# Optimization experiments

Hardware: AMD Instinct MI355X
Metric: run time of the kernel (lower is better)

## Reference

```python
import jax, jax.numpy as jnp
import numpy as np

B, L, D = 16, 512, 128
EPS = 1e-12


def _newton_schulz_1(S):
    # One Newton-Schulz orthogonalization iteration on batched [B,D,D] matrices:
    # X = S/||S||_F ; X <- 1.5*X - 0.5 * X @ X^T @ X
    norm = jnp.sqrt(jnp.sum(S * S, axis=(-2, -1), keepdims=True)) + 1e-6
    X = S / norm
    XXtX = jnp.einsum('bij,bkj,bkl->bil', X, X, X)
    return 1.5 * X - 0.5 * XXtX


def _poly(v, coeffs):
    # PolynomialFeatureLayer, degree 2, dimension-preserving:
    # phi(v) = c0*v + c1*v^2
    return coeffs[0] * v + coeffs[1] * v * v


def setup_inputs() -> dict:
    key = jax.random.key(0)
    ks = jax.random.split(key, 6)
    s = 1.0 / np.sqrt(D)
    x = jax.random.normal(ks[0], (B, L, D), jnp.float32)
    Wq = jax.random.normal(ks[1], (D, D), jnp.float32) * s
    Wk = jax.random.normal(ks[2], (D, D), jnp.float32) * s
    Wout = jax.random.normal(ks[3], (D, D), jnp.float32) * s
    bout = jnp.zeros((D,), jnp.float32)
    M0 = jax.random.normal(ks[4], (D, D), jnp.float32) * 0.01   # M_init
    S0 = jnp.zeros((D, D), jnp.float32)                          # S_init
    P0 = jnp.eye(D, dtype=jnp.float32) * 0.01                    # P_init
    log_gain = jnp.zeros((D,), jnp.float32)                      # QKProjectionLayer gain
    coeffs = jnp.array([1.0, 0.5], jnp.float32)                  # poly coeffs
    return {"x": x, "Wq": Wq, "Wk": Wk, "P0": P0, "M0": M0, "S0": S0,
            "log_gain": log_gain, "coeffs": coeffs, "Wout": Wout, "bout": bout}


def reference(x, Wq, Wk, P0, M0, S0, log_gain, coeffs, Wout, bout):
    b, l, d = x.shape
    q = jnp.einsum('bld,ed->ble', x, Wq)                 # q_proj (no bias)
    k = jnp.einsum('bld,ed->ble', x, Wk)                 # k_proj (no bias)
    k = k / jnp.maximum(jnp.linalg.norm(k, axis=-1, keepdims=True), EPS)  # F.normalize

    # QKProjectionLayer: rotate q by per-batch projection P, tanh gate with learned gain
    P = jnp.broadcast_to(P0, (b, d, d))
    gain = jnp.exp(log_gain)
    q_aligned = jnp.tanh(gain * jnp.einsum('bld,bde->ble', q, P))
    # (P_new = 0.99*P + 0.01*mean_t outer(q,k); state only, unused by output)

    k_phi = _poly(k, coeffs)
    q_phi = _poly(q_aligned, coeffs)

    M = jnp.broadcast_to(M0, (b, d, d))
    S = jnpp = jnp.broadcast_to(S0, (b, d, d))

    def step(carry, inputs):
        M, S = carry
        k_t, q_t, x_t = inputs                           # each [B,D]
        pred = jnp.einsum('bde,be->bd', M, k_t)
        err = pred - x_t
        S = 0.9 * S + err[:, :, None] * k_t[:, None, :]  # outer-product grad
        S_ortho = _newton_schulz_1(S)
        M = 0.99 * M - 0.01 * S_ortho
        y_t = jnp.einsum('bde,be->bd', M, q_t)
        return (M, S), y_t

    xs = (jnp.swapaxes(k_phi, 0, 1), jnp.swapaxes(q_phi, 0, 1), jnp.swapaxes(x, 0, 1))
    (_, _), ys = jax.lax.scan(step, (M, S), xs)          # ys: [L,B,D]
    stacked = jnp.swapaxes(ys, 0, 1)                     # [B,L,D]
    out = jnp.einsum('bld,ed->ble', stacked, Wout) + bout  # out_proj
    return out
```

## Files before the change

### kernel.cpp

```cpp
#include <hip/hip_runtime.h>

#define BB 16
#define LL 512
#define DD 128
#define CH 16
#define NCH (LL / CH)

typedef float v2f __attribute__((ext_vector_type(2)));
__device__ __forceinline__ v2f mk2(float x, float y) { v2f r; r.x = x; r.y = y; return r; }
__device__ __forceinline__ v2f fma2(v2f a, v2f b, v2f c) {
    return __builtin_elementwise_fma(a, b, c);
}

__device__ __forceinline__ float red8(float v) {
    v += __int_as_float(__builtin_amdgcn_update_dpp(
            0, __float_as_int(v), 0xB1, 0xF, 0xF, true));
    v += __int_as_float(__builtin_amdgcn_update_dpp(
            0, __float_as_int(v), 0x4E, 0xF, 0xF, true));
    v += __int_as_float(__builtin_amdgcn_update_dpp(
            0, __float_as_int(v), 0x141, 0xF, 0xF, true));
    return v;
}

#define SCAN_REGS __attribute__((amdgpu_waves_per_eu(2, 2)))

__global__ void transpose3_kernel(const float* __restrict__ Wq,
                                  const float* __restrict__ Wk,
                                  const float* __restrict__ Wout,
                                  float* __restrict__ WqT,
                                  float* __restrict__ WkT,
                                  float* __restrict__ WoutT) {
    const float* src; float* dst;
    if (blockIdx.x == 0)      { src = Wq;   dst = WqT;   }
    else if (blockIdx.x == 1) { src = Wk;   dst = WkT;   }
    else                      { src = Wout; dst = WoutT; }
    for (int idx = threadIdx.x; idx < DD * DD; idx += blockDim.x) {
        int r = idx >> 7, c = idx & 127;
        dst[c * DD + r] = src[idx];
    }
}

__global__ __launch_bounds__(128) void prologue_kernel(
        const float* __restrict__ x, const float* __restrict__ WqT,
        const float* __restrict__ WkT, const float* __restrict__ P0,
        const float* __restrict__ log_gain, const float* __restrict__ coeffs,
        float* __restrict__ kphi, float* __restrict__ qphi,
        float* __restrict__ cvt) {
    const int row0 = blockIdx.x * 8;
    const int e = threadIdx.x;
    __shared__ float xs[8][DD];
    __shared__ float qrow[8][DD];
    __shared__ float wred[8][2];
    __shared__ float cvred[8][2];

    #pragma unroll
    for (int rr = 0; rr < 8; ++rr)
        xs[rr][e] = x[(size_t)(row0 + rr) * DD + e];
    __syncthreads();

    float aq[8] = {0,0,0,0,0,0,0,0}, ak[8] = {0,0,0,0,0,0,0,0};
    #pragma unroll 4
    for (int d = 0; d < DD; ++d) {
        float wq = WqT[d * DD + e];
        float wk = WkT[d * DD + e];
        #pragma unroll
        for (int rr = 0; rr < 8; ++rr) {
            float xv = xs[rr][d];
            aq[rr] = fmaf(xv, wq, aq[rr]);
            ak[rr] = fmaf(xv, wk, ak[rr]);
        }
    }
    const int lane = threadIdx.x & 63, wv = threadIdx.x >> 6;
    #pragma unroll
    for (int rr = 0; rr < 8; ++rr) {
        float s = ak[rr] * ak[rr];
        #pragma unroll
        for (int m = 1; m <= 32; m <<= 1) s += __shfl_xor(s, m);
        if (lane == 0) wred[rr][wv] = s;
    }
    __syncthreads();
    const float c0 = coeffs[0], c1v = coeffs[1];
    #pragma unroll
    for (int rr = 0; rr < 8; ++rr) {
        float s = wred[rr][0] + wred[rr][1];
        float kn = ak[rr] / fmaxf(sqrtf(s), 1e-12f);
        float kv = c0 * kn + c1v * kn * kn;
        kphi[(size_t)(row0 + rr) * DD + e] = kv;
        float sq = kv * kv;
        #pragma unroll
        for (int m = 1; m <= 32; m <<= 1) sq += __shfl_xor(sq, m);
        if (lane == 0) cvred[rr][wv] = sq;
        qrow[rr][e] = aq[rr];
    }
    __syncthreads();
    if (e < 8) cvt[row0 + e] = cvred[e][0] + cvred[e][1];
    float acc[8] = {0,0,0,0,0,0,0,0};
    #pragma unroll 4
    for (int d = 0; d < DD; ++d) {
        float pv = P0[d * DD + e];
        #pragma unroll
        for (int rr = 0; rr < 8; ++rr) acc[rr] = fmaf(qrow[rr][d], pv, acc[rr]);
    }
    const float g = expf(log_gain[e]);
    #pragma unroll
    for (int rr = 0; rr < 8; ++rr) {
        float qa = tanhf(g * acc[rr]);
        qphi[(size_t)(row0 + rr) * DD + e] = c0 * qa + c1v * qa * qa;
    }
}


#define SCAN_STEP(SL, KKT, KKN)                                               \
  {                                                                           \
    const int so = (SL) * DD;                                                 \
    const float4 ft0 = *(const float4*)&ftab[(SL)][0];                        \
    const float4 ft1 = *(const float4*)&ftab[(SL)][4];                        \
    float4 pre0, pre1, pre2;                                                  \
    const bool doPre = ((SL) == 0) && (tc + 1 < NCH);                         \
    if (doPre) {                                                              \
      const size_t nbg = base + (size_t)(tc + 1) * CH * DD;                   \
      {                                                                       \
        int seg = w * 3 + 0, arr = seg >> 3, sub = seg & 7;                   \
        pre0 = *(const float4*)((arr == 0 ? kphi : (arr == 1 ? qphi : x))     \
                                + nbg + sub * 256 + lane * 4);                \
      }                                                                       \
      {                                                                       \
        int seg = w * 3 + 1, arr = seg >> 3, sub = seg & 7;                   \
        pre1 = *(const float4*)((arr == 0 ? kphi : (arr == 1 ? qphi : x))     \
                                + nbg + sub * 256 + lane * 4);                \
      }                                                                       \
      {                                                                       \
        int seg = w * 3 + 2, arr = seg >> 3, sub = seg & 7;                   \
        pre2 = *(const float4*)((arr == 0 ? kphi : (arr == 1 ? qphi : x))     \
                                + nbg + sub * 256 + lane * 4);                \
      }                                                                       \
    }                                                                         \
    v2f uu2[8], pa2[8];                                                       \
    {                                                                         \
      const float4* u4 = (const float4*)us;                                   \
      const float4* p4 = (const float4*)ps;                                   \
      _Pragma("unroll")                                                       \
      for (int m = 0; m < 4; ++m) {                                           \
        float4 a4 = u4[j + 8 * m], b4 = p4[j + 8 * m];                        \
        uu2[2*m]     = mk2(a4.x, a4.y);                                       \
        uu2[2*m + 1] = mk2(a4.z, a4.w);                                       \
        pa2[2*m]     = mk2(b4.x, b4.y);                                       \
        pa2[2*m + 1] = mk2(b4.z, b4.w);                                       \
      }                                                                       \
    }                                                                         \
    const float2 vc = *(const float2*)&kcb[so + r0];                          \
    const float vcxs = vc.x * ft0.y, vcys = vc.y * ft0.y;                     \
    const v2f vcx = mk2(vcxs, vcxs), vcy = mk2(vcys, vcys);                   \
    v2f w0v = mk2(0.f, 0.f), w1v = mk2(0.f, 0.f);                             \
    v2f h0v = mk2(0.f, 0.f), h1v = mk2(0.f, 0.f);                             \
    v2f cuv = mk2(0.f, 0.f), cupv = mk2(0.f, 0.f);                            \
    _Pragma("unroll")                                                         \
    for (int p = 0; p < 8; ++p) {                                             \
      v2f uv = uu2[p], pv = pa2[p];                                           \
      v2f st0 = ST2[p], st1 = ST2[8 + p];                                     \
      w0v  = fma2(st0, uv, w0v);                                              \
      w1v  = fma2(st1, uv, w1v);                                              \
      h0v  = fma2(st0, pv, h0v);                                              \
      h1v  = fma2(st1, pv, h1v);                                              \
      cuv  = fma2(uv, uv, cuv);                                               \
      cupv = fma2(uv, pv, cupv);                                              \
      ST2[p]     = fma2(vcx, uv, st0);                                        \
      ST2[8 + p] = fma2(vcy, uv, st1);                                        \
    }                                                                         \
    float w0 = red8(ft0.x * (w0v.x + w0v.y));                                 \
    float w1 = red8(ft0.x * (w1v.x + w1v.y));                                 \
    float h0 = red8(ft0.x * (h0v.x + h0v.y));                                 \
    float h1 = red8(ft0.x * (h1v.x + h1v.y));                                 \
    const float cu  = red8(cuv.x + cuv.y);                                    \
    const float cup = red8(cupv.x + cupv.y);                                  \
    n2 = a2v * n2 + 2.0f * a * cup + cu * cv;                                 \
       \
    const float nrm  = sqrtf(fmaxf(n2, 0.f)) + 1e-6f;                         \
    const float rn   = 1.0f / nrm;                                            \
    const float rn3  = rn * rn * rn;                                          \
    const float c1s  = rn * ft1.x;                                            \
    const float c2s  = rn3 * ft1.y;                                           \
    if (j == 0) {                                                             \
      *(float2*)&wsv[r0] = make_float2(w0, w1);                               \
      *(float2*)&hs[r0]  = make_float2(h0, h1);                               \
    }                                                                         \
    if (doPre) {                                                              \
      float* kn = kc[cb ^ 1]; float* qn = qc[cb ^ 1]; float* xn = xc[cb ^ 1]; \
      {                                                                       \
        int seg = w * 3 + 0, arr = seg >> 3, sub = seg & 7;                   \
        *(float4*)((arr == 0 ? kn : (arr == 1 ? qn : xn))                     \
                   + sub * 256 + lane * 4) = pre0;                            \
      }                                                                       \
      {                                                                       \
        int seg = w * 3 + 1, arr = seg >> 3, sub = seg & 7;                   \
        *(float4*)((arr == 0 ? kn : (arr == 1 ? qn : xn))                     \
                   + sub * 256 + lane * 4) = pre1;                            \
      }                                                                       \
      {                                                                       \
        int seg = w * 3 + 2, arr = seg >> 3, sub = seg & 7;                   \
        *(float4*)((arr == 0 ? kn : (arr == 1 ? qn : xn))                     \
                   + sub * 256 + lane * 4) = pre2;                            \
      }                                                                       \
    }                                                                         \
    __syncthreads();                                                          \
       \
    const float cvN = cvt[(size_t)b * LL + (size_t)(tc * CH + (SL) + 1)];     \
    v2f ww2[8];                                                               \
    v2f g0v = mk2(0.f, 0.f), g1v = mk2(0.f, 0.f);                             \
    {                                                                         \
      const float4* w4 = (const float4*)wsv;                                  \
      _Pragma("unroll")                                                       \
      for (int m = 0; m < 4; ++m) {                                           \
        float4 a4 = w4[j + 8 * m];                                            \
        v2f wv0 = mk2(a4.x, a4.y), wv1 = mk2(a4.z, a4.w);                     \
        ww2[2*m] = wv0; ww2[2*m + 1] = wv1;                                   \
        g0v = fma2(S2[2*m],     wv0, g0v);                                    \
        g0v = fma2(S2[2*m + 1], wv1, g0v);                                    \
        g1v = fma2(S2[8 + 2*m],     wv0, g1v);                                \
        g1v = fma2(S2[8 + 2*m + 1], wv1, g1v);                                \
      }                                                                       \
    }                                                                         \
    float g0 = red8(ft0.x * (g0v.x + g0v.y));                                 \
    float g1 = red8(ft0.x * (g1v.x + g1v.y));                                 \
    const float rho0 = a2v * g0 + a * cu * p0 + (a * cup + cv * cu) * u0;     \
    const float rho1 = a2v * g1 + a * cu * p1 + (a * cup + cv * cu) * u1;     \
    const float sg0  = a2v * p0 + a * cv * u0;                                \
    const float sg1  = a2v * p1 + a * cv * u1;                                \
    const float ta0  = a2v * u0, ta1 = a2v * u1;                              \
    const float f3i  = ft0.w;                                                 \
    const float u0p  = u0 * ft0.y, u1p = u1 * ft0.y;                          \
    const v2f u0v = mk2(u0p, u0p), u1v = mk2(u1p, u1p);                       \
    const v2f r0v = mk2(rho0 * f3i, rho0 * f3i);                              \
    const v2f r1v = mk2(rho1 * f3i, rho1 * f3i);                              \
    const v2f s0v = mk2(sg0 * f3i, sg0 * f3i);                                \
    const v2f s1v = mk2(sg1 * f3i, sg1 * f3i);                                \
    const v2f t0v = mk2(ta0 * f3i, ta0 * f3i);                                \
    const v2f t1v = mk2(ta1 * f3i, ta1 * f3i);                                \
    const v2f c1p = mk2(c1s, c1s), c2p = mk2(c2s, c2s);                       \
    const float* knb = ((SL) + 1 < CH) ? (kcb + so + DD) : kc[cb ^ 1];        \
    const float* xnb = ((SL) + 1 < CH) ? (xcb + so + DD) : xc[cb ^ 1];        \
    v2f y0v = mk2(0.f, 0.f), y1v = mk2(0.f, 0.f);                             \
    v2f pr0n = mk2(0.f, 0.f), pr1n = mk2(0.f, 0.f);                           \
    v2f pp0n = mk2(0.f, 0.f), pp1n = mk2(0.f, 0.f);                           \
    {                                                                         \
      const float4* h4  = (const float4*)hs;                                  \
      const float4* q4  = (const float4*)(qcb + so);                          \
      const float4* k4n = (const float4*)knb;                                 \
      _Pragma("unroll")                                                       \
      for (int m = 0; m < 4; ++m) {                                           \
        float4 b4  = h4[j + 8 * m];                                           \
        float4 c4v = q4[j + 8 * m];                                           \
        float4 k4v = k4n[j + 8 * m];                                          \
        v2f hv0 = mk2(b4.x, b4.y),   hv1 = mk2(b4.z, b4.w);                   \
        v2f qv0 = mk2(c4v.x, c4v.y), qv1 = mk2(c4v.z, c4v.w);                 \
        v2f kn0 = mk2(k4v.x, k4v.y), kn1 = mk2(k4v.z, k4v.w);                 \
        KKN[2*m] = kn0; KKN[2*m + 1] = kn1;                                   \
        v2f wv0 = ww2[2*m], wv1 = ww2[2*m + 1];                               \
        v2f kv0 = KKT[2*m], kv1 = KKT[2*m + 1];                               \
        v2f sn0 = fma2(u0v, kv0, S2[2*m]);                                    \
        v2f sn1 = fma2(u0v, kv1, S2[2*m + 1]);                                \
        S2[2*m] = sn0; S2[2*m + 1] = sn1;                                     \
        v2f an0 = fma2(r0v, kv0, fma2(s0v, wv0, fma2(t0v, hv0, A2[2*m])));    \
        v2f an1 = fma2(r0v, kv1, fma2(s0v, wv1, fma2(t0v, hv1, A2[2*m + 1])));\
        A2[2*m] = an0; A2[2*m + 1] = an1;                                     \
        v2f mn0 = fma2(c1p, sn0, fma2(c2p, an0, M2[2*m]));                    \
        v2f mn1 = fma2(c1p, sn1, fma2(c2p, an1, M2[2*m + 1]));                \
        M2[2*m] = mn0; M2[2*m + 1] = mn1;                                     \
        y0v  = fma2(mn0, qv0, y0v);                                           \
        y0v  = fma2(mn1, qv1, y0v);                                           \
        pr0n = fma2(mn0, kn0, pr0n);                                          \
        pr0n = fma2(mn1, kn1, pr0n);                                          \
        pp0n = fma2(sn0, kn0, pp0n);                                          \
        pp0n = fma2(sn1, kn1, pp0n);                                          \
        v2f sm0 = fma2(u1v, kv0, S2[8 + 2*m]);                                \
        v2f sm1 = fma2(u1v, kv1, S2[8 + 2*m + 1]);                            \
        S2[8 + 2*m] = sm0; S2[8 + 2*m + 1] = sm1;                             \
        v2f am0 = fma2(r1v, kv0, fma2(s1v, wv0, fma2(t1v, hv0, A2[8 + 2*m])));\
        v2f am1 = fma2(r1v, kv1,                                              \
                       fma2(s1v, wv1, fma2(t1v, hv1, A2[8 + 2*m + 1])));      \
        A2[8 + 2*m] = am0; A2[8 + 2*m + 1] = am1;                             \
        v2f mm0 = fma2(c1p, sm0, fma2(c2p, am0, M2[8 + 2*m]));                \
        v2f mm1 = fma2(c1p, sm1, fma2(c2p, am1, M2[8 + 2*m + 1]));            \
        M2[8 + 2*m] = mm0; M2[8 + 2*m + 1] = mm1;                             \
        y1v  = fma2(mm0, qv0, y1v);                                           \
        y1v  = fma2(mm1, qv1, y1v);                                           \
        pr1n = fma2(mm0, kn0, pr1n);                                          \
        pr1n = fma2(mm1, kn1, pr1n);                                          \
        pp1n = fma2(sm0, kn0, pp1n);                                          \
        pp1n = fma2(sm1, kn1, pp1n);                                          \
      }                                                                       \
    }                                                                         \
    float y0 = red8(ft1.z * (y0v.x + y0v.y));                                 \
    float y1 = red8(ft1.z * (y1v.x + y1v.y));                                 \
    if (j == 0)                                                               \
      *(float2*)&yc[so + r0] = make_float2(y0, y1);                           \
    const float2 xn = *(const float2*)&xnb[r0];                               \
    u0 = red8(fmaf(ft1.z, pr0n.x + pr0n.y, -0.125f * xn.x));                  \
    u1 = red8(fmaf(ft1.z, pr1n.x + pr1n.y, -0.125f * xn.y));                  \
    p0 = red8(ft0.z * (pp0n.x + pp0n.y));                                     \
    p1 = red8(ft0.z * (pp1n.x + pp1n.y));                                     \
    cv = cvN;                                                                 \
    if (j == 0) {                                                             \
      *(float2*)&us[r0] = make_float2(u0, u1);                                \
      *(float2*)&ps[r0] = make_float2(p0, p1);                                \
    }                                                                         \
    __syncthreads();                                                          \
  }

__global__ SCAN_REGS __launch_bounds__(512)
void scan_kernel(
        const float* __restrict__ kphi, const float* __restrict__ qphi,
        const float* __restrict__ x, const float* __restrict__ M0,
        const float* __restrict__ S0, float* __restrict__ ys,
        const float* __restrict__ cvt) {
    const int b    = blockIdx.x;
    const int tid  = threadIdx.x;
    const int j    = tid & 7;
    const int g    = tid >> 3;
    const int r0   = 2 * g;
    const int w    = tid >> 6;
    const int lane = tid & 63;

    __shared__ __align__(16) float kc[2][CH * DD];
    __shared__ __align__(16) float qc[2][CH * DD];
    __shared__ __align__(16) float xc[2][CH * DD];
    __shared__ __align__(16) float yc[CH * DD];
    __shared__ __align__(16) float us[DD], ps[DD], wsv[DD], hs[DD];
    __shared__ __align__(16) float ftab[CH][8];
    __shared__ float red[64];
    __shared__ float n2sh;

    {
        const float ia  = 1.0f / 0.9f;
        const float ia3 = ia * ia * ia;
        const float ra  = 0.9f / 0.99f;
        const float ra3 = 0.729f / 0.99f;
        float faS = 1.f, faiS = 1.f, fa3iS = 1.f;
        float q1S = -0.015f, q3S = 0.005f, fmS = 1.f;
        #pragma unroll 1
        for (int s = 0; s < CH; ++s) {
            float faN = faS * 0.9f;
            faiS *= ia; fa3iS *= ia3; q1S *= ra; q3S *= ra3; fmS *= 0.99f;
            if (tid == 0) {
                ftab[s][0] = faS;   ftab[s][1] = faiS;
                ftab[s][2] = faN;   ftab[s][3] = fa3iS;
                ftab[s][4] = q1S;   ftab[s][5] = q3S;
                ftab[s][6] = fmS;   ftab[s][7] = 0.f;
            }
            faS = faN;
        }
    }
    const float a2c = 0.9f * 0.9f, a4c = a2c * a2c, a8c = a4c * a4c;
    const float fa16 = a8c * a8c;
    const float fa48 = fa16 * fa16 * fa16;
    const float p2c = 0.99f * 0.99f, p4c = p2c * p2c, p8c = p4c * p4c;
    const float pm16 = p8c * p8c;

    v2f S2[16], ST2[16], A2[16], M2[16];
    {
        const float4* S04 = (const float4*)S0;
        const float4* M04 = (const float4*)M0;
        #pragma unroll
        for (int rl = 0; rl < 2; ++rl)
            #pragma unroll
            for (int m = 0; m < 4; ++m) {
                int f4 = (r0 + rl) * 32 + j + 8 * m;
                float4 s4 = S04[f4], m4 = M04[f4];
                int p = rl * 8 + 2 * m;
                S2[p]     = mk2(s4.x, s4.y);
                S2[p + 1] = mk2(s4.z, s4.w);
                M2[p]     = mk2(m4.x, m4.y);
                M2[p + 1] = mk2(m4.z, m4.w);
            }
        #pragma unroll
        for (int rl = 0; rl < 2; ++rl)
            #pragma unroll
            for (int m = 0; m < 4; ++m) {
                int p = rl * 8 + 2 * m;
                ST2[p]     = mk2(S0[(size_t)(4*j + 32*m + 0) * DD + r0 + rl],
                                 S0[(size_t)(4*j + 32*m + 1) * DD + r0 + rl]);
                ST2[p + 1] = mk2(S0[(size_t)(4*j + 32*m + 2) * DD + r0 + rl],
                                 S0[(size_t)(4*j + 32*m + 3) * DD + r0 + rl]);
            }
        #pragma unroll
        for (int p = 0; p < 16; ++p) A2[p] = mk2(0.f, 0.f);
    }

    float sp = 0.f;
    #pragma unroll
    for (int p = 0; p < 16; ++p) {
        sp = fmaf(S2[p].x, S2[p].x, sp);
        sp = fmaf(S2[p].y, S2[p].y, sp);
    }
    sp = red8(sp);
    if (j == 0) red[g] = sp;

    const size_t base = (size_t)b * LL * DD;

    #pragma unroll
    for (int i = 0; i < 3; ++i) {
        int seg = w * 3 + i, arr = seg >> 3, sub = seg & 7;
        const float* sp0 = (arr == 0 ? kphi : (arr == 1 ? qphi : x))
                           + base + sub * 256 + lane * 4;
        float* dp = (arr == 0 ? kc[0] : (arr == 1 ? qc[0] : xc[0]))
                    + sub * 256 + lane * 4;
        *(float4*)dp = *(const float4*)sp0;
    }
    __syncthreads();
    if (tid < 64) {
        float s = red[tid];
        #pragma unroll
        for (int m = 1; m <= 32; m <<= 1) s += __shfl_xor(s, m);
        if (tid == 0) n2sh = s;
    }
    __syncthreads();
    float n2 = n2sh;

    const float a = 0.9f, a2v = 0.81f;

    v2f kk2[8], kkn[8];
    float u0, u1, p0, p1, cv;
    {
        const float4* k4 = (const float4*)kc[0];
        v2f pr0v = mk2(0.f, 0.f), pr1v = mk2(0.f, 0.f);
        v2f pp0v = mk2(0.f, 0.f), pp1v = mk2(0.f, 0.f);
        v2f cvv  = mk2(0.f, 0.f);
        #pragma unroll
        for (int m = 0; m < 4; ++m) {
            float4 v4 = k4[j + 8 * m];
            v2f k0 = mk2(v4.x, v4.y), k1 = mk2(v4.z, v4.w);
            kk2[2*m] = k0; kk2[2*m + 1] = k1;
            pr0v = fma2(M2[2*m],     k0, pr0v);
            pr0v = fma2(M2[2*m + 1], k1, pr0v);
            pr1v = fma2(M2[8 + 2*m],     k0, pr1v);
            pr1v = fma2(M2[8 + 2*m + 1], k1, pr1v);
            pp0v = fma2(S2[2*m],     k0, pp0v);
            pp0v = fma2(S2[2*m + 1], k1, pp0v);
            pp1v = fma2(S2[8 + 2*m],     k0, pp1v);
            pp1v = fma2(S2[8 + 2*m + 1], k1, pp1v);
            cvv  = fma2(k0, k0, cvv);
            cvv  = fma2(k1, k1, cvv);
        }
        float pr0 = red8(pr0v.x + pr0v.y);
        float pr1 = red8(pr1v.x + pr1v.y);
        p0 = red8(pp0v.x + pp0v.y);
        p1 = red8(pp1v.x + pp1v.y);
        cv = red8(cvv.x + cvv.y);
        const float2 xv = *(const float2*)&xc[0][r0];
        u0 = pr0 - xv.x; u1 = pr1 - xv.y;
        if (j == 0) {
            *(float2*)&us[r0] = make_float2(u0, u1);
            *(float2*)&ps[r0] = make_float2(p0, p1);
        }
    }
    __syncthreads();

    #pragma unroll 1
    for (int tc = 0; tc < NCH; ++tc) {
        const int cb = tc & 1;
        const float* kcb = kc[cb];
        const float* qcb = qc[cb];
        const float* xcb = xc[cb];

        #pragma unroll 1
        for (int sl2 = 0; sl2 < CH; sl2 += 2) {
            SCAN_STEP(sl2,     kk2, kkn)
            SCAN_STEP(sl2 + 1, kkn, kk2)
        }

        float4 yv = *(float4*)&yc[tid * 4];
        *(float4*)(ys + base + (size_t)tc * CH * DD + tid * 4) = yv;

        if (tc + 1 < NCH) {
            const v2f rs = mk2(fa16, fa16);
            const v2f rA = mk2(fa48, fa48);
            const v2f rM = mk2(pm16, pm16);
            #pragma unroll
            for (int p = 0; p < 16; ++p) {
                S2[p] *= rs; ST2[p] *= rs; A2[p] *= rA; M2[p] *= rM;
            }
        }
    }
}

#undef SCAN_STEP

__global__ __launch_bounds__(128) void epilogue_kernel(
        const float* __restrict__ ys, const float* __restrict__ WoutT,
        const float* __restrict__ bout, float* __restrict__ out) {
    const int row0 = blockIdx.x * 8;
    const int e = threadIdx.x;
    __shared__ float yr[8][DD];
    #pragma unroll
    for (int rr = 0; rr < 8; ++rr)
        yr[rr][e] = ys[(size_t)(row0 + rr) * DD + e];
    __syncthreads();
    float acc[8] = {0,0,0,0,0,0,0,0};
    #pragma unroll 4
    for (int d = 0; d < DD; ++d) {
        float w = WoutT[d * DD + e];
        #pragma unroll
        for (int rr = 0; rr < 8; ++rr) acc[rr] = fmaf(yr[rr][d], w, acc[rr]);
    }
    const float bo = bout[e];
    #pragma unroll
    for (int rr = 0; rr < 8; ++rr)
        out[(size_t)(row0 + rr) * DD + e] = acc[rr] + bo;
}

extern "C" void kernel_launch(void* const* d_in, const int* in_sizes, int n_in,
                              void* d_out, int out_size, void* d_ws, size_t ws_size,
                              hipStream_t stream) {
    const float* x        = (const float*)d_in[0];
    const float* Wq       = (const float*)d_in[1];
    const float* Wk       = (const float*)d_in[2];
    const float* P0       = (const float*)d_in[3];
    const float* M0       = (const float*)d_in[4];
    const float* S0       = (const float*)d_in[5];
    const float* log_gain = (const float*)d_in[6];
    const float* coeffs   = (const float*)d_in[7];
    const float* Wout     = (const float*)d_in[8];
    const float* bout     = (const float*)d_in[9];
    float* out = (float*)d_out;

    float* ws    = (float*)d_ws;
    float* WqT   = ws;
    float* WkT   = ws + 16384;
    float* WoutT = ws + 32768;
    float* kphi  = ws + 49152;
    float* qphi  = kphi + (size_t)BB * LL * DD;
    float* ysb   = qphi + (size_t)BB * LL * DD;
    float* cvt   = ysb  + (size_t)BB * LL * DD;

    hipLaunchKernelGGL(transpose3_kernel, dim3(3), dim3(256), 0, stream,
                       Wq, Wk, Wout, WqT, WkT, WoutT);
    hipLaunchKernelGGL(prologue_kernel, dim3(BB * LL / 8), dim3(128), 0, stream,
                       x, WqT, WkT, P0, log_gain, coeffs, kphi, qphi, cvt);
    hipLaunchKernelGGL(scan_kernel, dim3(BB), dim3(512), 0, stream,
                       kphi, qphi, x, M0, S0, ysb, cvt);
    hipLaunchKernelGGL(epilogue_kernel, dim3(BB * LL / 8), dim3(128), 0, stream,
                       ysb, WoutT, bout, out);
}
```

Baseline: 1.062 ms.

## Halve scan block size, give each thread four state rows

The scan kernel now runs 256 threads per batch instead of 512, and each thread owns four rows of the S, ST, A and M state instead of two. The per-step loops, reductions, prefetch segments and ys stores are rewritten to match, and the waves-per-EU hint drops to 1 so more registers are available. The goal is to cut barrier and shared-memory exchange cost per step and to get more instruction-level parallelism per lane. In exchange, register pressure doubles, which risks spills, and fewer waves are left to hide latency.

```diff
diff --git a/kernel.cpp b/kernel.cpp
--- a/kernel.cpp
+++ b/kernel.cpp
@@ -22,7 +22,7 @@
     return v;
 }
 
-#define SCAN_REGS __attribute__((amdgpu_waves_per_eu(2, 2)))
+#define SCAN_REGS __attribute__((amdgpu_waves_per_eu(1, 1)))
 
 __global__ void transpose3_kernel(const float* __restrict__ Wq,
                                   const float* __restrict__ Wk,
@@ -115,24 +115,15 @@
     const int so = (SL) * DD;                                                 \
     const float4 ft0 = *(const float4*)&ftab[(SL)][0];                        \
     const float4 ft1 = *(const float4*)&ftab[(SL)][4];                        \
-    float4 pre0, pre1, pre2;                                                  \
+    float4 pre[6];                                                            \
     const bool doPre = ((SL) == 0) && (tc + 1 < NCH);                         \
     if (doPre) {                                                              \
       const size_t nbg = base + (size_t)(tc + 1) * CH * DD;                   \
-      {                                                                       \
-        int seg = w * 3 + 0, arr = seg >> 3, sub = seg & 7;                   \
-        pre0 = *(const float4*)((arr == 0 ? kphi : (arr == 1 ? qphi : x))     \
-                                + nbg + sub * 256 + lane * 4);                \
-      }                                                                       \
-      {                                                                       \
-        int seg = w * 3 + 1, arr = seg >> 3, sub = seg & 7;                   \
-        pre1 = *(const float4*)((arr == 0 ? kphi : (arr == 1 ? qphi : x))     \
-                                + nbg + sub * 256 + lane * 4);                \
-      }                                                                       \
-      {                                                                       \
-        int seg = w * 3 + 2, arr = seg >> 3, sub = seg & 7;                   \
-        pre2 = *(const float4*)((arr == 0 ? kphi : (arr == 1 ? qphi : x))     \
-                                + nbg + sub * 256 + lane * 4);                \
+      _Pragma("unroll")                                                       \
+      for (int i = 0; i < 6; ++i) {                                           \
+        int seg = w * 6 + i, arr = seg >> 3, sub = seg & 7;                   \
+        pre[i] = *(const float4*)((arr == 0 ? kphi : (arr == 1 ? qphi : x))   \
+                                  + nbg + sub * 256 + lane * 4);              \
       }                                                                       \
     }                                                                         \
     v2f uu2[8], pa2[8];                                                       \
@@ -148,65 +139,63 @@
         pa2[2*m + 1] = mk2(b4.z, b4.w);                                       \
       }                                                                       \
     }                                                                         \
-    const float2 vc = *(const float2*)&kcb[so + r0];                          \
-    const float vcxs = vc.x * ft0.y, vcys = vc.y * ft0.y;                     \
-    const v2f vcx = mk2(vcxs, vcxs), vcy = mk2(vcys, vcys);                   \
-    v2f w0v = mk2(0.f, 0.f), w1v = mk2(0.f, 0.f);                             \
-    v2f h0v = mk2(0.f, 0.f), h1v = mk2(0.f, 0.f);                             \
+    const float4 vc = *(const float4*)&kcb[so + r0];                          \
+    v2f vcb[4];                                                               \
+    vcb[0] = mk2(vc.x * ft0.y, vc.x * ft0.y);                                 \
+    vcb[1] = mk2(vc.y * ft0.y, vc.y * ft0.y);                                 \
+    vcb[2] = mk2(vc.z * ft0.y, vc.z * ft0.y);                                 \
+    vcb[3] = mk2(vc.w * ft0.y, vc.w * ft0.y);                                 \
+    v2f wAv[4], hAv[4];                                                       \
+    _Pragma("unroll")                                                         \
+    for (int rl = 0; rl < 4; ++rl) { wAv[rl] = mk2(0.f, 0.f);                 \
+                                     hAv[rl] = mk2(0.f, 0.f); }               \
     v2f cuv = mk2(0.f, 0.f), cupv = mk2(0.f, 0.f);                            \
     _Pragma("unroll")                                                         \
     for (int p = 0; p < 8; ++p) {                                             \
       v2f uv = uu2[p], pv = pa2[p];                                           \
-      v2f st0 = ST2[p], st1 = ST2[8 + p];                                     \
-      w0v  = fma2(st0, uv, w0v);                                              \
-      w1v  = fma2(st1, uv, w1v);                                              \
-      h0v  = fma2(st0, pv, h0v);                                              \
-      h1v  = fma2(st1, pv, h1v);                                              \
+      _Pragma("unroll")                                                       \
+      for (int rl = 0; rl < 4; ++rl) {                                        \
+        v2f st = ST2[rl*8 + p];                                               \
+        wAv[rl] = fma2(st, uv, wAv[rl]);                                      \
+        hAv[rl] = fma2(st, pv, hAv[rl]);                                      \
+        ST2[rl*8 + p] = fma2(vcb[rl], uv, st);                                \
+      }                                                                       \
       cuv  = fma2(uv, uv, cuv);                                               \
       cupv = fma2(uv, pv, cupv);                                              \
-      ST2[p]     = fma2(vcx, uv, st0);                                        \
-      ST2[8 + p] = fma2(vcy, uv, st1);                                        \
-    }                                                                         \
-    float w0 = red8(ft0.x * (w0v.x + w0v.y));                                 \
-    float w1 = red8(ft0.x * (w1v.x + w1v.y));                                 \
-    float h0 = red8(ft0.x * (h0v.x + h0v.y));                                 \
-    float h1 = red8(ft0.x * (h1v.x + h1v.y));                                 \
+    }                                                                         \
+    float wr[4], hr[4];                                                       \
+    _Pragma("unroll")                                                         \
+    for (int rl = 0; rl < 4; ++rl) {                                          \
+      wr[rl] = red8(ft0.x * (wAv[rl].x + wAv[rl].y));                         \
+      hr[rl] = red8(ft0.x * (hAv[rl].x + hAv[rl].y));                         \
+    }                                                                         \
     const float cu  = red8(cuv.x + cuv.y);                                    \
     const float cup = red8(cupv.x + cupv.y);                                  \
     n2 = a2v * n2 + 2.0f * a * cup + cu * cv;                                 \
-       \
     const float nrm  = sqrtf(fmaxf(n2, 0.f)) + 1e-6f;                         \
     const float rn   = 1.0f / nrm;                                            \
     const float rn3  = rn * rn * rn;                                          \
     const float c1s  = rn * ft1.x;                                            \
     const float c2s  = rn3 * ft1.y;                                           \
     if (j == 0) {                                                             \
-      *(float2*)&wsv[r0] = make_float2(w0, w1);                               \
-      *(float2*)&hs[r0]  = make_float2(h0, h1);                               \
+      *(float4*)&wsv[r0] = make_float4(wr[0], wr[1], wr[2], wr[3]);           \
+      *(float4*)&hs[r0]  = make_float4(hr[0], hr[1], hr[2], hr[3]);           \
     }                                                                         \
     if (doPre) {                                                              \
       float* kn = kc[cb ^ 1]; float* qn = qc[cb ^ 1]; float* xn = xc[cb ^ 1]; \
-      {                                                                       \
-        int seg = w * 3 + 0, arr = seg >> 3, sub = seg & 7;                   \
+      _Pragma("unroll")                                                       \
+      for (int i = 0; i < 6; ++i) {                                           \
+        int seg = w * 6 + i, arr = seg >> 3, sub = seg & 7;                   \
         *(float4*)((arr == 0 ? kn : (arr == 1 ? qn : xn))                     \
-                   + sub * 256 + lane * 4) = pre0;                            \
+                   + sub * 256 + lane * 4) = pre[i];                          \
       }                                                                       \
-      {                                                                       \
-        int seg = w * 3 + 1, arr = seg >> 3, sub = seg & 7;                   \
-        *(float4*)((arr == 0 ? kn : (arr == 1 ? qn : xn))                     \
-                   + sub * 256 + lane * 4) = pre1;                            \
-      }                                                                       \
-      {                                                                       \
-        int seg = w * 3 + 2, arr = seg >> 3, sub = seg & 7;                   \
-        *(float4*)((arr == 0 ? kn : (arr == 1 ? qn : xn))                     \
-                   + sub * 256 + lane * 4) = pre2;                            \
-      }                                                                       \
     }                                                                         \
     __syncthreads();                                                          \
-       \
     const float cvN = cvt[(size_t)b * LL + (size_t)(tc * CH + (SL) + 1)];     \
     v2f ww2[8];                                                               \
-    v2f g0v = mk2(0.f, 0.f), g1v = mk2(0.f, 0.f);                             \
+    v2f gAv[4];                                                               \
+    _Pragma("unroll")                                                         \
+    for (int rl = 0; rl < 4; ++rl) gAv[rl] = mk2(0.f, 0.f);                   \
     {                                                                         \
       const float4* w4 = (const float4*)wsv;                                  \
       _Pragma("unroll")                                                       \
@@ -214,34 +203,35 @@
         float4 a4 = w4[j + 8 * m];                                            \
         v2f wv0 = mk2(a4.x, a4.y), wv1 = mk2(a4.z, a4.w);                     \
         ww2[2*m] = wv0; ww2[2*m + 1] = wv1;                                   \
-        g0v = fma2(S2[2*m],     wv0, g0v);                                    \
-        g0v = fma2(S2[2*m + 1], wv1, g0v);                                    \
-        g1v = fma2(S2[8 + 2*m],     wv0, g1v);                                \
-        g1v = fma2(S2[8 + 2*m + 1], wv1, g1v);                                \
+        _Pragma("unroll")                                                     \
+        for (int rl = 0; rl < 4; ++rl) {                                      \
+          gAv[rl] = fma2(S2[rl*8 + 2*m],     wv0, gAv[rl]);                   \
+          gAv[rl] = fma2(S2[rl*8 + 2*m + 1], wv1, gAv[rl]);                   \
+        }                                                                     \
       }                                                                       \
     }                                                                         \
-    float g0 = red8(ft0.x * (g0v.x + g0v.y));                                 \
-    float g1 = red8(ft0.x * (g1v.x + g1v.y));                                 \
-    const float rho0 = a2v * g0 + a * cu * p0 + (a * cup + cv * cu) * u0;     \
-    const float rho1 = a2v * g1 + a * cu * p1 + (a * cup + cv * cu) * u1;     \
-    const float sg0  = a2v * p0 + a * cv * u0;                                \
-    const float sg1  = a2v * p1 + a * cv * u1;                                \
-    const float ta0  = a2v * u0, ta1 = a2v * u1;                              \
-    const float f3i  = ft0.w;                                                 \
-    const float u0p  = u0 * ft0.y, u1p = u1 * ft0.y;                          \
-    const v2f u0v = mk2(u0p, u0p), u1v = mk2(u1p, u1p);                       \
-    const v2f r0v = mk2(rho0 * f3i, rho0 * f3i);                              \
-    const v2f r1v = mk2(rho1 * f3i, rho1 * f3i);                              \
-    const v2f s0v = mk2(sg0 * f3i, sg0 * f3i);                                \
-    const v2f s1v = mk2(sg1 * f3i, sg1 * f3i);                                \
-    const v2f t0v = mk2(ta0 * f3i, ta0 * f3i);                                \
-    const v2f t1v = mk2(ta1 * f3i, ta1 * f3i);                                \
+    const float f3i = ft0.w;                                                  \
+    v2f uB[4], rB[4], sB[4], tB[4];                                           \
+    _Pragma("unroll")                                                         \
+    for (int rl = 0; rl < 4; ++rl) {                                          \
+      float gr  = red8(ft0.x * (gAv[rl].x + gAv[rl].y));                      \
+      float rho = a2v * gr + a * cu * p_[rl] + (a * cup + cv * cu) * u_[rl];  \
+      float sg  = a2v * p_[rl] + a * cv * u_[rl];                             \
+      float ta  = a2v * u_[rl];                                               \
+      uB[rl] = mk2(u_[rl] * ft0.y, u_[rl] * ft0.y);                           \
+      rB[rl] = mk2(rho * f3i, rho * f3i);                                     \
+      sB[rl] = mk2(sg * f3i, sg * f3i);                                       \
+      tB[rl] = mk2(ta * f3i, ta * f3i);                                       \
+    }                                                                         \
     const v2f c1p = mk2(c1s, c1s), c2p = mk2(c2s, c2s);                       \
     const float* knb = ((SL) + 1 < CH) ? (kcb + so + DD) : kc[cb ^ 1];        \
     const float* xnb = ((SL) + 1 < CH) ? (xcb + so + DD) : xc[cb ^ 1];        \
-    v2f y0v = mk2(0.f, 0.f), y1v = mk2(0.f, 0.f);                             \
-    v2f pr0n = mk2(0.f, 0.f), pr1n = mk2(0.f, 0.f);                           \
-    v2f pp0n = mk2(0.f, 0.f), pp1n = mk2(0.f, 0.f);                           \
+    v2f yv[4], prv[4], ppv[4];                                                \
+    _Pragma("unroll")                                                         \
+    for (int rl = 0; rl < 4; ++rl) {                                          \
+      yv[rl] = mk2(0.f, 0.f); prv[rl] = mk2(0.f, 0.f);                        \
+      ppv[rl] = mk2(0.f, 0.f);                                                \
+    }                                                                         \
     {                                                                         \
       const float4* h4  = (const float4*)hs;                                  \
       const float4* q4  = (const float4*)(qcb + so);                          \
@@ -257,57 +247,55 @@
         KKN[2*m] = kn0; KKN[2*m + 1] = kn1;                                   \
         v2f wv0 = ww2[2*m], wv1 = ww2[2*m + 1];                               \
         v2f kv0 = KKT[2*m], kv1 = KKT[2*m + 1];                               \
-        v2f sn0 = fma2(u0v, kv0, S2[2*m]);                                    \
-        v2f sn1 = fma2(u0v, kv1, S2[2*m + 1]);                                \
-        S2[2*m] = sn0; S2[2*m + 1] = sn1;                                     \
-        v2f an0 = fma2(r0v, kv0, fma2(s0v, wv0, fma2(t0v, hv0, A2[2*m])));    \
-        v2f an1 = fma2(r0v, kv1, fma2(s0v, wv1, fma2(t0v, hv1, A2[2*m + 1])));\
-        A2[2*m] = an0; A2[2*m + 1] = an1;                                     \
-        v2f mn0 = fma2(c1p, sn0, fma2(c2p, an0, M2[2*m]));                    \
-        v2f mn1 = fma2(c1p, sn1, fma2(c2p, an1, M2[2*m + 1]));                \
-        M2[2*m] = mn0; M2[2*m + 1] = mn1;                                     \
-        y0v  = fma2(mn0, qv0, y0v);                                           \
-        y0v  = fma2(mn1, qv1, y0v);                                           \
-        pr0n = fma2(mn0, kn0, pr0n);                                          \
-        pr0n = fma2(mn1, kn1, pr0n);                                          \
-        pp0n = fma2(sn0, kn0, pp0n);                                          \
-        pp0n = fma2(sn1, kn1, pp0n);                                          \
-        v2f sm0 = fma2(u1v, kv0, S2[8 + 2*m]);                                \
-        v2f sm1 = fma2(u1v, kv1, S2[8 + 2*m + 1]);                            \
-        S2[8 + 2*m] = sm0; S2[8 + 2*m + 1] = sm1;                             \
-        v2f am0 = fma2(r1v, kv0, fma2(s1v, wv0, fma2(t1v, hv0, A2[8 + 2*m])));\
-        v2f am1 = fma2(r1v, kv1,                                              \
-                       fma2(s1v, wv1, fma2(t1v, hv1, A2[8 + 2*m + 1])));      \
-        A2[8 + 2*m] = am0; A2[8 + 2*m + 1] = am1;                             \
-        v2f mm0 = fma2(c1p, sm0, fma2(c2p, am0, M2[8 + 2*m]));                \
-        v2f mm1 = fma2(c1p, sm1, fma2(c2p, am1, M2[8 + 2*m + 1]));            \
-        M2[8 + 2*m] = mm0; M2[8 + 2*m + 1] = mm1;                             \
-        y1v  = fma2(mm0, qv0, y1v);                                           \
-        y1v  = fma2(mm1, qv1, y1v);                                           \
-        pr1n = fma2(mm0, kn0, pr1n);                                          \
-        pr1n = fma2(mm1, kn1, pr1n);                                          \
-        pp1n = fma2(sm0, kn0, pp1n);                                          \
-        pp1n = fma2(sm1, kn1, pp1n);                                          \
+        _Pragma("unroll")                                                     \
+        for (int rl = 0; rl < 4; ++rl) {                                      \
+          v2f sn0 = fma2(uB[rl], kv0, S2[rl*8 + 2*m]);                        \
+          v2f sn1 = fma2(uB[rl], kv1, S2[rl*8 + 2*m + 1]);                    \
+          S2[rl*8 + 2*m] = sn0; S2[rl*8 + 2*m + 1] = sn1;                     \
+          v2f an0 = fma2(rB[rl], kv0,                                         \
+                         fma2(sB[rl], wv0, fma2(tB[rl], hv0,                  \
+                                                A2[rl*8 + 2*m])));            \
+          v2f an1 = fma2(rB[rl], kv1,                                         \
+                         fma2(sB[rl], wv1, fma2(tB[rl], hv1,                  \
+                                                A2[rl*8 + 2*m + 1])));        \
+          A2[rl*8 + 2*m] = an0; A2[rl*8 + 2*m + 1] = an1;                     \
+          v2f mn0 = fma2(c1p, sn0, fma2(c2p, an0, M2[rl*8 + 2*m]));           \
+          v2f mn1 = fma2(c1p, sn1, fma2(c2p, an1, M2[rl*8 + 2*m + 1]));       \
+          M2[rl*8 + 2*m] = mn0; M2[rl*8 + 2*m + 1] = mn1;                     \
+          yv[rl]  = fma2(mn0, qv0, yv[rl]);                                   \
+          yv[rl]  = fma2(mn1, qv1, yv[rl]);                                   \
+          prv[rl] = fma2(mn0, kn0, prv[rl]);                                  \
+          prv[rl] = fma2(mn1, kn1, prv[rl]);                                  \
+          ppv[rl] = fma2(sn0, kn0, ppv[rl]);                                  \
+          ppv[rl] = fma2(sn1, kn1, ppv[rl]);                                  \
+        }                                                                     \
       }                                                                       \
     }                                                                         \
-    float y0 = red8(ft1.z * (y0v.x + y0v.y));                                 \
-    float y1 = red8(ft1.z * (y1v.x + y1v.y));                                 \
-    if (j == 0)                                                               \
-      *(float2*)&yc[so + r0] = make_float2(y0, y1);                           \
-    const float2 xn = *(const float2*)&xnb[r0];                               \
-    u0 = red8(fmaf(ft1.z, pr0n.x + pr0n.y, -0.125f * xn.x));                  \
-    u1 = red8(fmaf(ft1.z, pr1n.x + pr1n.y, -0.125f * xn.y));                  \
-    p0 = red8(ft0.z * (pp0n.x + pp0n.y));                                     \
-    p1 = red8(ft0.z * (pp1n.x + pp1n.y));                                     \
+    {                                                                         \
+      float yr0 = red8(ft1.z * (yv[0].x + yv[0].y));                          \
+      float yr1 = red8(ft1.z * (yv[1].x + yv[1].y));                          \
+      float yr2 = red8(ft1.z * (yv[2].x + yv[2].y));                          \
+      float yr3 = red8(ft1.z * (yv[3].x + yv[3].y));                          \
+      if (j == 0)                                                             \
+        *(float4*)&yc[so + r0] = make_float4(yr0, yr1, yr2, yr3);             \
+    }                                                                         \
+    const float4 xn = *(const float4*)&xnb[r0];                               \
+    float xnA[4]; xnA[0] = xn.x; xnA[1] = xn.y;                               \
+    xnA[2] = xn.z; xnA[3] = xn.w;                                             \
+    _Pragma("unroll")                                                         \
+    for (int rl = 0; rl < 4; ++rl) {                                          \
+      u_[rl] = red8(fmaf(ft1.z, prv[rl].x + prv[rl].y, -0.125f * xnA[rl]));   \
+      p_[rl] = red8(ft0.z * (ppv[rl].x + ppv[rl].y));                         \
+    }                                                                         \
     cv = cvN;                                                                 \
     if (j == 0) {                                                             \
-      *(float2*)&us[r0] = make_float2(u0, u1);                                \
-      *(float2*)&ps[r0] = make_float2(p0, p1);                                \
+      *(float4*)&us[r0] = make_float4(u_[0], u_[1], u_[2], u_[3]);            \
+      *(float4*)&ps[r0] = make_float4(p_[0], p_[1], p_[2], p_[3]);            \
     }                                                                         \
     __syncthreads();                                                          \
   }
 
-__global__ SCAN_REGS __launch_bounds__(512)
+__global__ SCAN_REGS __launch_bounds__(256)
 void scan_kernel(
         const float* __restrict__ kphi, const float* __restrict__ qphi,
         const float* __restrict__ x, const float* __restrict__ M0,
@@ -317,7 +305,7 @@
     const int tid  = threadIdx.x;
     const int j    = tid & 7;
     const int g    = tid >> 3;
-    const int r0   = 2 * g;
+    const int r0   = 4 * g;
     const int w    = tid >> 6;
     const int lane = tid & 63;
 
@@ -327,7 +315,7 @@
     __shared__ __align__(16) float yc[CH * DD];
     __shared__ __align__(16) float us[DD], ps[DD], wsv[DD], hs[DD];
     __shared__ __align__(16) float ftab[CH][8];
-    __shared__ float red[64];
+    __shared__ float red[32];
     __shared__ float n2sh;
 
     {
@@ -356,12 +344,12 @@
     const float p2c = 0.99f * 0.99f, p4c = p2c * p2c, p8c = p4c * p4c;
     const float pm16 = p8c * p8c;
 
-    v2f S2[16], ST2[16], A2[16], M2[16];
+    v2f S2[32], ST2[32], A2[32], M2[32];
     {
         const float4* S04 = (const float4*)S0;
         const float4* M04 = (const float4*)M0;
         #pragma unroll
-        for (int rl = 0; rl < 2; ++rl)
+        for (int rl = 0; rl < 4; ++rl)
             #pragma unroll
             for (int m = 0; m < 4; ++m) {
                 int f4 = (r0 + rl) * 32 + j + 8 * m;
@@ -373,7 +361,7 @@
                 M2[p + 1] = mk2(m4.z, m4.w);
             }
         #pragma unroll
-        for (int rl = 0; rl < 2; ++rl)
+        for (int rl = 0; rl < 4; ++rl)
             #pragma unroll
             for (int m = 0; m < 4; ++m) {
                 int p = rl * 8 + 2 * m;
@@ -383,12 +371,12 @@
                                  S0[(size_t)(4*j + 32*m + 3) * DD + r0 + rl]);
             }
         #pragma unroll
-        for (int p = 0; p < 16; ++p) A2[p] = mk2(0.f, 0.f);
+        for (int p = 0; p < 32; ++p) A2[p] = mk2(0.f, 0.f);
     }
 
     float sp = 0.f;
     #pragma unroll
-    for (int p = 0; p < 16; ++p) {
+    for (int p = 0; p < 32; ++p) {
         sp = fmaf(S2[p].x, S2[p].x, sp);
         sp = fmaf(S2[p].y, S2[p].y, sp);
     }
@@ -398,8 +386,8 @@
     const size_t base = (size_t)b * LL * DD;
 
     #pragma unroll
-    for (int i = 0; i < 3; ++i) {
-        int seg = w * 3 + i, arr = seg >> 3, sub = seg & 7;
+    for (int i = 0; i < 6; ++i) {
+        int seg = w * 6 + i, arr = seg >> 3, sub = seg & 7;
         const float* sp0 = (arr == 0 ? kphi : (arr == 1 ? qphi : x))
                            + base + sub * 256 + lane * 4;
         float* dp = (arr == 0 ? kc[0] : (arr == 1 ? qc[0] : xc[0]))
@@ -407,10 +395,10 @@
         *(float4*)dp = *(const float4*)sp0;
     }
     __syncthreads();
-    if (tid < 64) {
+    if (tid < 32) {
         float s = red[tid];
         #pragma unroll
-        for (int m = 1; m <= 32; m <<= 1) s += __shfl_xor(s, m);
+        for (int m = 1; m <= 16; m <<= 1) s += __shfl_xor(s, m);
         if (tid == 0) n2sh = s;
     }
     __syncthreads();
@@ -419,38 +407,42 @@
     const float a = 0.9f, a2v = 0.81f;
 
     v2f kk2[8], kkn[8];
-    float u0, u1, p0, p1, cv;
+    float u_[4], p_[4], cv;
     {
         const float4* k4 = (const float4*)kc[0];
-        v2f pr0v = mk2(0.f, 0.f), pr1v = mk2(0.f, 0.f);
-        v2f pp0v = mk2(0.f, 0.f), pp1v = mk2(0.f, 0.f);
-        v2f cvv  = mk2(0.f, 0.f);
+        v2f prA[4], ppA[4];
+        #pragma unroll
+        for (int rl = 0; rl < 4; ++rl) {
+            prA[rl] = mk2(0.f, 0.f); ppA[rl] = mk2(0.f, 0.f);
+        }
+        v2f cvv = mk2(0.f, 0.f);
         #pragma unroll
         for (int m = 0; m < 4; ++m) {
             float4 v4 = k4[j + 8 * m];
             v2f k0 = mk2(v4.x, v4.y), k1 = mk2(v4.z, v4.w);
             kk2[2*m] = k0; kk2[2*m + 1] = k1;
-            pr0v = fma2(M2[2*m],     k0, pr0v);
-            pr0v = fma2(M2[2*m + 1], k1, pr0v);
-            pr1v = fma2(M2[8 + 2*m],     k0, pr1v);
-            pr1v = fma2(M2[8 + 2*m + 1], k1, pr1v);
-            pp0v = fma2(S2[2*m],     k0, pp0v);
-            pp0v = fma2(S2[2*m + 1], k1, pp0v);
-            pp1v = fma2(S2[8 + 2*m],     k0, pp1v);
-            pp1v = fma2(S2[8 + 2*m + 1], k1, pp1v);
-            cvv  = fma2(k0, k0, cvv);
-            cvv  = fma2(k1, k1, cvv);
-        }
-        float pr0 = red8(pr0v.x + pr0v.y);
-        float pr1 = red8(pr1v.x + pr1v.y);
-        p0 = red8(pp0v.x + pp0v.y);
-        p1 = red8(pp1v.x + pp1v.y);
+            #pragma unroll
+            for (int rl = 0; rl < 4; ++rl) {
+                prA[rl] = fma2(M2[rl*8 + 2*m],     k0, prA[rl]);
+                prA[rl] = fma2(M2[rl*8 + 2*m + 1], k1, prA[rl]);
+                ppA[rl] = fma2(S2[rl*8 + 2*m],     k0, ppA[rl]);
+                ppA[rl] = fma2(S2[rl*8 + 2*m + 1], k1, ppA[rl]);
+            }
+            cvv = fma2(k0, k0, cvv);
+            cvv = fma2(k1, k1, cvv);
+        }
         cv = red8(cvv.x + cvv.y);
-        const float2 xv = *(const float2*)&xc[0][r0];
-        u0 = pr0 - xv.x; u1 = pr1 - xv.y;
+        const float4 xv = *(const float4*)&xc[0][r0];
+        float xvA[4]; xvA[0] = xv.x; xvA[1] = xv.y; xvA[2] = xv.z; xvA[3] = xv.w;
+        #pragma unroll
+        for (int rl = 0; rl < 4; ++rl) {
+            float pr = red8(prA[rl].x + prA[rl].y);
+            p_[rl] = red8(ppA[rl].x + ppA[rl].y);
+            u_[rl] = pr - xvA[rl];
+        }
         if (j == 0) {
-            *(float2*)&us[r0] = make_float2(u0, u1);
-            *(float2*)&ps[r0] = make_float2(p0, p1);
+            *(float4*)&us[r0] = make_float4(u_[0], u_[1], u_[2], u_[3]);
+            *(float4*)&ps[r0] = make_float4(p_[0], p_[1], p_[2], p_[3]);
         }
     }
     __syncthreads();
@@ -468,15 +460,20 @@
             SCAN_STEP(sl2 + 1, kkn, kk2)
         }
 
-        float4 yv = *(float4*)&yc[tid * 4];
-        *(float4*)(ys + base + (size_t)tc * CH * DD + tid * 4) = yv;
+        {
+            float4 yv1 = *(float4*)&yc[tid * 8];
+            float4 yv2 = *(float4*)&yc[tid * 8 + 4];
+            float* dst = ys + base + (size_t)tc * CH * DD + tid * 8;
+            *(float4*)dst = yv1;
+            *(float4*)(dst + 4) = yv2;
+        }
 
         if (tc + 1 < NCH) {
             const v2f rs = mk2(fa16, fa16);
             const v2f rA = mk2(fa48, fa48);
             const v2f rM = mk2(pm16, pm16);
             #pragma unroll
-            for (int p = 0; p < 16; ++p) {
+            for (int p = 0; p < 32; ++p) {
                 S2[p] *= rs; ST2[p] *= rs; A2[p] *= rA; M2[p] *= rM;
             }
         }
@@ -536,7 +533,7 @@
                        Wq, Wk, Wout, WqT, WkT, WoutT);
     hipLaunchKernelGGL(prologue_kernel, dim3(BB * LL / 8), dim3(128), 0, stream,
                        x, WqT, WkT, P0, log_gain, coeffs, kphi, qphi, cvt);
-    hipLaunchKernelGGL(scan_kernel, dim3(BB), dim3(512), 0, stream,
+    hipLaunchKernelGGL(scan_kernel, dim3(BB), dim3(256), 0, stream,
                        kphi, qphi, x, M0, S0, ysb, cvt);
     hipLaunchKernelGGL(epilogue_kernel, dim3(BB * LL / 8), dim3(128), 0, stream,
                        ysb, WoutT, bout, out);
```

Result: slower. 1.474 ms (+38.7%).
